# Optimization experiments

Measured on AMD Instinct MI355X. Metric: run time of the kernel, lower is better.

## Reference

```python
import jax, jax.numpy as jnp
import numpy as np

N_ATOMS = 10000
N_EDGES = 250000
F_DIM = 128
N_RBF = 20
CUTOFF = 5.0
N_INT = 3
EPS = 1e-8


def setup_inputs() -> dict:
    key = jax.random.key(0)
    ks = jax.random.split(key, 16)
    inp = {}
    inp["atomic_numbers"] = jax.random.randint(ks[0], (N_ATOMS,), 1, 101)
    # positions in a 5 Angstrom box so many pairs lie inside the cutoff
    inp["R"] = jax.random.uniform(ks[1], (N_ATOMS, 3), dtype=jnp.float32) * 5.0
    idx_i = jnp.sort(jax.random.randint(ks[2], (N_EDGES,), 0, N_ATOMS))
    # ensure idx_j != idx_i so d_ij > 0
    idx_j = (idx_i + 1 + jax.random.randint(ks[3], (N_EDGES,), 0, N_ATOMS - 1)) % N_ATOMS
    inp["idx_i"] = idx_i
    inp["idx_j"] = idx_j
    inp["offsets"] = jnp.zeros((N_EDGES, 3), dtype=jnp.float32)

    def w(k, shape):
        fan_in = shape[-2]
        return jax.random.normal(k, shape, dtype=jnp.float32) / np.sqrt(fan_in).astype(np.float32)

    inp["emb"] = jax.random.normal(ks[4], (101, F_DIM), dtype=jnp.float32)
    inp["filt_W"] = w(ks[5], (N_RBF, 3 * F_DIM))
    inp["filt_b"] = jax.random.normal(ks[6], (3 * F_DIM,), dtype=jnp.float32) * 0.01
    inp["int_W1"] = w(ks[7], (N_INT, F_DIM, F_DIM))
    inp["int_b1"] = jnp.zeros((N_INT, 1, F_DIM), dtype=jnp.float32)
    inp["int_W2"] = w(ks[8], (N_INT, F_DIM, 3 * F_DIM))
    inp["int_b2"] = jnp.zeros((N_INT, 1, 3 * F_DIM), dtype=jnp.float32)
    inp["mix_Wmu"] = w(ks[9], (N_INT, F_DIM, 2 * F_DIM))
    inp["mix_W1"] = w(ks[10], (N_INT, 2 * F_DIM, F_DIM))
    inp["mix_b1"] = jnp.zeros((N_INT, 1, F_DIM), dtype=jnp.float32)
    inp["mix_W2"] = w(ks[11], (N_INT, F_DIM, 3 * F_DIM))
    inp["mix_b2"] = jnp.zeros((N_INT, 1, 3 * F_DIM), dtype=jnp.float32)
    return inp


def painn_forward(atomic_numbers, idx_i, idx_j, R, offsets, emb, filt_W, filt_b,
                  int_W1, int_b1, int_W2, int_b2,
                  mix_Wmu, mix_W1, mix_b1, mix_W2, mix_b2):
    n_atoms = atomic_numbers.shape[0]
    # geometry
    r_ij = R[idx_j] - R[idx_i] + offsets                      # [E,3]
    d_ij = jnp.linalg.norm(r_ij, axis=1, keepdims=True)       # [E,1]
    dir_ij = r_ij / d_ij                                      # [E,3]
    # Gaussian radial basis + cosine cutoff (schnetpack defaults)
    centers = jnp.linspace(0.0, CUTOFF, N_RBF, dtype=jnp.float32)
    coeff = -0.5 / (centers[1] - centers[0]) ** 2
    phi = jnp.exp(coeff * (d_ij[..., None] - centers) ** 2)   # [E,1,N_RBF]
    fcut = 0.5 * (jnp.cos(d_ij * (jnp.pi / CUTOFF)) + 1.0) * (d_ij < CUTOFF)  # [E,1]
    Wij = (phi @ filt_W + filt_b) * fcut[..., None]           # [E,1,3F] (shared filters)

    q = emb[atomic_numbers][:, None, :]                       # [N,1,F]
    mu = jnp.zeros((n_atoms, 3, F_DIM), dtype=q.dtype)        # [N,3,F]

    for i in range(N_INT):
        # ---- interaction (equivariant message passing) ----
        x = jax.nn.silu(q @ int_W1[i] + int_b1[i]) @ int_W2[i] + int_b2[i]  # [N,1,3F]
        xj = x[idx_j]                                          # [E,1,3F]
        muj = mu[idx_j]                                        # [E,3,F]
        xw = Wij * xj                                          # [E,1,3F]
        dq, dmuR, dmumu = jnp.split(xw, 3, axis=-1)            # each [E,1,F]
        dq = jax.ops.segment_sum(dq, idx_i, num_segments=n_atoms)          # [N,1,F]
        dmu = dmuR * dir_ij[..., None] + dmumu * muj           # [E,3,F]
        dmu = jax.ops.segment_sum(dmu, idx_i, num_segments=n_atoms)        # [N,3,F]
        q = q + dq
        mu = mu + dmu
        # ---- mixing (intra-atomic) ----
        mu_mix = mu @ mix_Wmu[i]                               # [N,3,2F]
        mu_V, mu_W = jnp.split(mu_mix, 2, axis=-1)             # [N,3,F] each
        mu_Vn = jnp.sqrt(jnp.sum(mu_V ** 2, axis=-2, keepdims=True) + EPS)  # [N,1,F]
        ctx = jnp.concatenate([q, mu_Vn], axis=-1)             # [N,1,2F]
        xm = jax.nn.silu(ctx @ mix_W1[i] + mix_b1[i]) @ mix_W2[i] + mix_b2[i]  # [N,1,3F]
        dq_intra, dmu_intra, dqmu_intra = jnp.split(xm, 3, axis=-1)
        dmu_intra = dmu_intra * mu_W                           # [N,3,F]
        dqmu_intra = dqmu_intra * jnp.sum(mu_V * mu_W, axis=1, keepdims=True)  # [N,1,F]
        q = q + dq_intra + dqmu_intra
        mu = mu + dmu_intra

    return q.squeeze(1), mu                                    # [N,F], [N,3,F]


def reference(atomic_numbers, R, idx_i, idx_j, offsets, emb, filt_W, filt_b,
              int_W1, int_b1, int_W2, int_b2,
              mix_Wmu, mix_W1, mix_b1, mix_W2, mix_b2):
    return painn_forward(atomic_numbers, idx_i, idx_j, R, offsets, emb, filt_W, filt_b,
                         int_W1, int_b1, int_W2, int_b2,
                         mix_Wmu, mix_W1, mix_b1, mix_W2, mix_b2)
```

## Files before the change

### kernel.cpp

```cpp
#include <hip/hip_runtime.h>
#include <math.h>

#define NA 10000
#define NE 250000
#define FD 128
#define NRBF 20
#define RCUT 5.0f

typedef _Float16 h16;
typedef __attribute__((ext_vector_type(8))) _Float16 half8;
typedef __attribute__((ext_vector_type(2))) _Float16 half2v;
typedef __attribute__((ext_vector_type(4))) float f32x4;

static __device__ __forceinline__ half8 f32x8_to_h8(const float* p) {
    float4 a = *(const float4*)p;
    float4 b = *(const float4*)(p + 4);
    half8 r;
    r[0] = (h16)a.x; r[1] = (h16)a.y; r[2] = (h16)a.z; r[3] = (h16)a.w;
    r[4] = (h16)b.x; r[5] = (h16)b.y; r[6] = (h16)b.z; r[7] = (h16)b.w;
    return r;
}
static __device__ __forceinline__ float silu(float v) {
    return v / (1.f + expf(-v));
}

__global__ __launch_bounds__(256) void setup_kernel(
    const float* __restrict__ R, const int* __restrict__ idx_i,
    const int* __restrict__ idx_j, const float* __restrict__ offsets,
    float* __restrict__ dir, h16* __restrict__ ph, int* __restrict__ row_start,
    const float* __restrict__ int_W1, const float* __restrict__ int_W2,
    const float* __restrict__ mix_Wmu, const float* __restrict__ mix_W1,
    const float* __restrict__ mix_W2,
    h16* __restrict__ W1t, h16* __restrict__ W2t, h16* __restrict__ WmuT,
    h16* __restrict__ mW1t, h16* __restrict__ mW2t,
    const float* __restrict__ filt_W, const float* __restrict__ filt_b,
    h16* __restrict__ fwt)
{
    const int b = blockIdx.x;
    if (b < 977) {
        int e = b * 256 + threadIdx.x;
        if (e >= NE) return;
        int i = idx_i[e], j = idx_j[e];
        float rx = R[j * 3 + 0] - R[i * 3 + 0] + offsets[e * 3 + 0];
        float ry = R[j * 3 + 1] - R[i * 3 + 1] + offsets[e * 3 + 1];
        float rz = R[j * 3 + 2] - R[i * 3 + 2] + offsets[e * 3 + 2];
        float d = sqrtf(rx * rx + ry * ry + rz * rz);
        float inv = 1.f / d;
        float fcut = 0.f;
        if (d < RCUT) fcut = 0.5f * (cosf(d * (3.14159265358979323846f / RCUT)) + 1.f);
        *(float4*)&dir[(size_t)e * 4] = make_float4(rx * inv, ry * inv, rz * inv, 0.f);
        h16* pp = ph + (size_t)e * 32;
        const float delta = RCUT / 19.f;
        const float coeff = -0.5f / (delta * delta);
#pragma unroll
        for (int r = 0; r < NRBF; ++r) {
            float dc = d - (float)r * delta;
            pp[r] = (h16)(expf(coeff * dc * dc) * fcut);
        }
        pp[20] = (h16)fcut;
#pragma unroll
        for (int r = 21; r < 32; ++r) pp[r] = (h16)0.f;
    } else if (b < 1017) {
        int n = (b - 977) * 256 + threadIdx.x;
        if (n > NA) return;
        int lo = 0, hi = NE;
        while (lo < hi) {
            int mid = (lo + hi) >> 1;
            if (idx_i[mid] < n) lo = mid + 1; else hi = mid;
        }
        row_start[n] = lo;
    } else {
        int idx = (b - 1017) * 256 + threadIdx.x;
        if (idx < 49152) {
            int bt = idx >> 14, rem = idx & 16383;
            int nn = rem >> 7, kk = rem & 127;
            W1t[idx] = (h16)int_W1[(size_t)bt * 16384 + kk * 128 + nn];
        } else if ((idx -= 49152) < 147456) {
            int bt = idx / 49152, rem = idx - bt * 49152;
            int nn = rem >> 7, kk = rem & 127;
            W2t[idx] = (h16)int_W2[(size_t)bt * 49152 + kk * 384 + nn];
        } else if ((idx -= 147456) < 98304) {
            int bt = idx >> 15, rem = idx & 32767;
            int nn = rem >> 7, kk = rem & 127;
            WmuT[idx] = (h16)mix_Wmu[(size_t)bt * 32768 + kk * 256 + nn];
        } else if ((idx -= 98304) < 98304) {
            int bt = idx >> 15, rem = idx & 32767;
            int nn = rem >> 8, kk = rem & 255;
            mW1t[idx] = (h16)mix_W1[(size_t)bt * 32768 + kk * 128 + nn];
        } else if ((idx -= 98304) < 147456) {
            int bt = idx / 49152, rem = idx - bt * 49152;
            int nn = rem >> 7, kk = rem & 127;
            mW2t[idx] = (h16)mix_W2[(size_t)bt * 49152 + kk * 384 + nn];
        } else if ((idx -= 147456) < 12288) {
            int nn = idx >> 5, kk = idx & 31;
            float v = 0.f;
            if (kk < 20) v = filt_W[kk * 384 + nn];
            else if (kk == 20) v = filt_b[nn];
            fwt[idx] = (h16)v;
        }
    }
}

__global__ __launch_bounds__(256) void intmlp0_kernel(
    const int* __restrict__ Z, const float* __restrict__ emb, float* __restrict__ q,
    const h16* __restrict__ W1t, const float* __restrict__ b1,
    const h16* __restrict__ W2t, const float* __restrict__ b2, h16* __restrict__ x16)
{
    __shared__ h16 Hs[16 * 136];
    const int tid = threadIdx.x;
    const int wave = tid >> 6, lane = tid & 63;
    const int ar = lane & 15, kg = lane >> 4;
    const size_t row0 = (size_t)blockIdx.x * 16;

    {
        int a = tid >> 4, f0 = (tid & 15) * 8;
        const float* src = emb + (size_t)Z[row0 + a] * 128 + f0;
        float4 v0 = *(const float4*)src;
        float4 v1 = *(const float4*)(src + 4);
        *(float4*)&q[(row0 + a) * 128 + f0] = v0;
        *(float4*)&q[(row0 + a) * 128 + f0 + 4] = v1;
    }
    const int zr = Z[row0 + ar];
    f32x4 a1[2] = {};
    for (int ks = 0; ks < 128; ks += 32) {
        int k = ks + kg * 8;
        half8 af = f32x8_to_h8(emb + (size_t)zr * 128 + k);
#pragma unroll
        for (int tt = 0; tt < 2; ++tt) {
            int t = wave * 2 + tt;
            half8 bf = *(const half8*)&W1t[(size_t)(t * 16 + ar) * 128 + k];
            a1[tt] = __builtin_amdgcn_mfma_f32_16x16x32_f16(af, bf, a1[tt], 0, 0, 0);
        }
    }
#pragma unroll
    for (int tt = 0; tt < 2; ++tt) {
        int col = (wave * 2 + tt) * 16 + ar;
        float bb = b1[col];
#pragma unroll
        for (int r = 0; r < 4; ++r)
            Hs[(kg * 4 + r) * 136 + col] = (h16)silu(a1[tt][r] + bb);
    }
    __syncthreads();
    f32x4 a2[6] = {};
    for (int ks = 0; ks < 128; ks += 32) {
        int k = ks + kg * 8;
        half8 af = *(const half8*)&Hs[ar * 136 + k];
#pragma unroll
        for (int tt = 0; tt < 6; ++tt) {
            int t = wave * 6 + tt;
            half8 bf = *(const half8*)&W2t[(size_t)(t * 16 + ar) * 128 + k];
            a2[tt] = __builtin_amdgcn_mfma_f32_16x16x32_f16(af, bf, a2[tt], 0, 0, 0);
        }
    }
#pragma unroll
    for (int tt = 0; tt < 6; ++tt) {
        int col = (wave * 6 + tt) * 16 + ar;
        float bb = b2[col];
#pragma unroll
        for (int r = 0; r < 4; ++r)
            x16[(row0 + kg * 4 + r) * 384 + col] = (h16)(a2[tt][r] + bb);
    }
}

template<bool HAS_MU>
__global__ __launch_bounds__(128) void edge_kernel(
    const float* __restrict__ dir, const h16* __restrict__ ph,
    const h16* __restrict__ fwt,
    const int* __restrict__ row_start, const int* __restrict__ idx_j,
    const h16* __restrict__ x16, const h16* __restrict__ mu16p,
    const float* __restrict__ mup, float* __restrict__ mun,
    h16* __restrict__ mu16n, float* __restrict__ q)
{
    const int n = blockIdx.x, f = threadIdx.x;
    half2v fa[12], fb[12], fc[12];
    {
        const half8* pa = (const half8*)(fwt + (size_t)f * 32);
        const half8* pb = (const half8*)(fwt + (size_t)(128 + f) * 32);
#pragma unroll
        for (int r = 0; r < 3; ++r) {
            *(half8*)&fa[r * 4] = pa[r];
            *(half8*)&fb[r * 4] = pb[r];
        }
        if (HAS_MU) {
            const half8* pc = (const half8*)(fwt + (size_t)(256 + f) * 32);
#pragma unroll
            for (int r = 0; r < 3; ++r)
                *(half8*)&fc[r * 4] = pc[r];
        }
    }
    float accq = 0.f, am0 = 0.f, am1 = 0.f, am2 = 0.f;
    const int e0 = row_start[n], e1 = row_start[n + 1];
    for (int e = e0; e < e1; ++e) {
        half2v pr[12];
        const h16* pb8 = ph + (size_t)e * 32;
        *(half8*)&pr[0] = *(const half8*)pb8;
        *(half8*)&pr[4] = *(const half8*)(pb8 + 8);
        *(half8*)&pr[8] = *(const half8*)(pb8 + 16);
        half2v A0 = {(h16)0.f, (h16)0.f}, A1 = A0, A2 = A0;
#pragma unroll
        for (int r = 0; r < 11; ++r) {
            A0 = pr[r] * fa[r] + A0;
            A1 = pr[r] * fb[r] + A1;
            if (HAS_MU) A2 = pr[r] * fc[r] + A2;
        }
        float w0 = (float)A0[0] + (float)A0[1];
        float w1 = (float)A1[0] + (float)A1[1];
        int j = idx_j[e];
        float4 g = *(const float4*)&dir[(size_t)e * 4];
        const h16* xb = x16 + (size_t)j * 384;
        float x0 = (float)xb[f], x1 = (float)xb[128 + f];
        accq = fmaf(w0, x0, accq);
        float xw1 = w1 * x1;
        if (HAS_MU) {
            float w2 = (float)A2[0] + (float)A2[1];
            float x2 = (float)xb[256 + f];
            float xw2 = w2 * x2;
            const h16* mb = mu16p + (size_t)j * 384;
            am0 += xw1 * g.x + xw2 * (float)mb[f];
            am1 += xw1 * g.y + xw2 * (float)mb[128 + f];
            am2 += xw1 * g.z + xw2 * (float)mb[256 + f];
        } else {
            am0 = fmaf(xw1, g.x, am0);
            am1 = fmaf(xw1, g.y, am1);
            am2 = fmaf(xw1, g.z, am2);
        }
    }
    q[(size_t)n * FD + f] += accq;
    size_t b = (size_t)n * 384;
    float m0 = (HAS_MU ? mup[b + f] : 0.f) + am0;
    float m1 = (HAS_MU ? mup[b + 128 + f] : 0.f) + am1;
    float m2 = (HAS_MU ? mup[b + 256 + f] : 0.f) + am2;
    mun[b + f] = m0; mun[b + 128 + f] = m1; mun[b + 256 + f] = m2;
    mu16n[b + f] = (h16)m0; mu16n[b + 128 + f] = (h16)m1; mu16n[b + 256 + f] = (h16)m2;
}

__global__ __launch_bounds__(256) void mixint_kernel(
    const h16* __restrict__ mu16n, const h16* __restrict__ WmuT,
    const h16* __restrict__ W1t, const float* __restrict__ b1,
    const h16* __restrict__ W2t, const float* __restrict__ b2,
    float* __restrict__ q, float* __restrict__ mu, h16* __restrict__ mu16w,
    const h16* __restrict__ nW1t, const float* __restrict__ nb1,
    const h16* __restrict__ nW2t, const float* __restrict__ nb2,
    h16* __restrict__ x16)
{
    __shared__ h16 MM[48 * 264];
    __shared__ h16 CT[16 * 264];
    __shared__ h16 Hs[16 * 136];
    __shared__ h16 XM[16 * 392];
    const int tid = threadIdx.x;
    const int wave = tid >> 6, lane = tid & 63;
    const int ar = lane & 15, kg = lane >> 4;
    const size_t row0 = (size_t)blockIdx.x * 16;

    {
        f32x4 acc[3][4] = {};
        int aloc[3], dloc[3];
#pragma unroll
        for (int rt = 0; rt < 3; ++rt) {
            int rr = rt * 16 + ar;
            aloc[rt] = rr / 3;
            dloc[rt] = rr - 3 * aloc[rt];
        }
        for (int ks = 0; ks < 128; ks += 32) {
            int k = ks + kg * 8;
            half8 afr[3];
#pragma unroll
            for (int rt = 0; rt < 3; ++rt)
                afr[rt] = *(const half8*)&mu16n[(row0 + aloc[rt]) * 384 + dloc[rt] * 128 + k];
#pragma unroll
            for (int ct = 0; ct < 4; ++ct) {
                int cc = wave * 4 + ct;
                half8 bf = *(const half8*)&WmuT[(size_t)(cc * 16 + ar) * 128 + k];
#pragma unroll
                for (int rt = 0; rt < 3; ++rt)
                    acc[rt][ct] = __builtin_amdgcn_mfma_f32_16x16x32_f16(afr[rt], bf, acc[rt][ct], 0, 0, 0);
            }
        }
#pragma unroll
        for (int rt = 0; rt < 3; ++rt)
#pragma unroll
            for (int ct = 0; ct < 4; ++ct) {
                int col = (wave * 4 + ct) * 16 + ar;
#pragma unroll
                for (int r = 0; r < 4; ++r)
                    MM[(rt * 16 + kg * 4 + r) * 264 + col] = (h16)acc[rt][ct][r];
            }
    }
    __syncthreads();

    {
        int a = tid >> 4, fi = (tid & 15) * 8;
        const float* qp = q + (row0 + a) * 128 + fi;
        float4 q0 = *(const float4*)qp;
        float4 q1 = *(const float4*)(qp + 4);
        float qv[8] = {q0.x, q0.y, q0.z, q0.w, q1.x, q1.y, q1.z, q1.w};
#pragma unroll
        for (int jj = 0; jj < 8; ++jj) {
            int ff = fi + jj;
            float v0 = (float)MM[(a * 3 + 0) * 264 + ff];
            float v1 = (float)MM[(a * 3 + 1) * 264 + ff];
            float v2 = (float)MM[(a * 3 + 2) * 264 + ff];
            CT[a * 264 + 128 + ff] = (h16)sqrtf(v0 * v0 + v1 * v1 + v2 * v2 + 1e-8f);
            CT[a * 264 + ff] = (h16)qv[jj];
        }
    }
    __syncthreads();

    {
        f32x4 a1[2] = {};
        for (int ks = 0; ks < 256; ks += 32) {
            int k = ks + kg * 8;
            half8 af = *(const half8*)&CT[ar * 264 + k];
#pragma unroll
            for (int tt = 0; tt < 2; ++tt) {
                int t = wave * 2 + tt;
                half8 bf = *(const half8*)&W1t[(size_t)(t * 16 + ar) * 256 + k];
                a1[tt] = __builtin_amdgcn_mfma_f32_16x16x32_f16(af, bf, a1[tt], 0, 0, 0);
            }
        }
#pragma unroll
        for (int tt = 0; tt < 2; ++tt) {
            int col = (wave * 2 + tt) * 16 + ar;
            float bb = b1[col];
#pragma unroll
            for (int r = 0; r < 4; ++r)
                Hs[(kg * 4 + r) * 136 + col] = (h16)silu(a1[tt][r] + bb);
        }
    }
    __syncthreads();

    {
        f32x4 a2[6] = {};
        for (int ks = 0; ks < 128; ks += 32) {
            int k = ks + kg * 8;
            half8 af = *(const half8*)&Hs[ar * 136 + k];
#pragma unroll
            for (int tt = 0; tt < 6; ++tt) {
                int t = wave * 6 + tt;
                half8 bf = *(const half8*)&W2t[(size_t)(t * 16 + ar) * 128 + k];
                a2[tt] = __builtin_amdgcn_mfma_f32_16x16x32_f16(af, bf, a2[tt], 0, 0, 0);
            }
        }
#pragma unroll
        for (int tt = 0; tt < 6; ++tt) {
            int col = (wave * 6 + tt) * 16 + ar;
            float bb = b2[col];
#pragma unroll
            for (int r = 0; r < 4; ++r)
                XM[(kg * 4 + r) * 392 + col] = (h16)(a2[tt][r] + bb);
        }
    }
    __syncthreads();

    {
        int a = tid >> 4, fi = (tid & 15) * 8;
        size_t n = row0 + a;
#pragma unroll
        for (int jj = 0; jj < 8; ++jj) {
            int ff = fi + jj;
            float dq  = (float)XM[a * 392 + ff];
            float dm  = (float)XM[a * 392 + 128 + ff];
            float dqm = (float)XM[a * 392 + 256 + ff];
            float v0 = (float)MM[(a * 3 + 0) * 264 + ff], w0 = (float)MM[(a * 3 + 0) * 264 + 128 + ff];
            float v1 = (float)MM[(a * 3 + 1) * 264 + ff], w1 = (float)MM[(a * 3 + 1) * 264 + 128 + ff];
            float v2 = (float)MM[(a * 3 + 2) * 264 + ff], w2 = (float)MM[(a * 3 + 2) * 264 + 128 + ff];
            float sv = v0 * w0 + v1 * w1 + v2 * w2;
            float qn = q[n * 128 + ff] + dq + dqm * sv;
            q[n * 128 + ff] = qn;
            CT[a * 264 + ff] = (h16)qn;
            size_t b = n * 384 + ff;
            float m0 = mu[b] + dm * w0;
            float m1 = mu[b + 128] + dm * w1;
            float m2 = mu[b + 256] + dm * w2;
            mu[b] = m0; mu[b + 128] = m1; mu[b + 256] = m2;
            mu16w[b] = (h16)m0; mu16w[b + 128] = (h16)m1; mu16w[b + 256] = (h16)m2;
        }
    }
    if (!nW1t) return;
    __syncthreads();

    {
        f32x4 a1[2] = {};
        for (int ks = 0; ks < 128; ks += 32) {
            int k = ks + kg * 8;
            half8 af = *(const half8*)&CT[ar * 264 + k];
#pragma unroll
            for (int tt = 0; tt < 2; ++tt) {
                int t = wave * 2 + tt;
                half8 bf = *(const half8*)&nW1t[(size_t)(t * 16 + ar) * 128 + k];
                a1[tt] = __builtin_amdgcn_mfma_f32_16x16x32_f16(af, bf, a1[tt], 0, 0, 0);
            }
        }
#pragma unroll
        for (int tt = 0; tt < 2; ++tt) {
            int col = (wave * 2 + tt) * 16 + ar;
            float bb = nb1[col];
#pragma unroll
            for (int r = 0; r < 4; ++r)
                Hs[(kg * 4 + r) * 136 + col] = (h16)silu(a1[tt][r] + bb);
        }
        __syncthreads();
        f32x4 a2[6] = {};
        for (int ks = 0; ks < 128; ks += 32) {
            int k = ks + kg * 8;
            half8 af = *(const half8*)&Hs[ar * 136 + k];
#pragma unroll
            for (int tt = 0; tt < 6; ++tt) {
                int t = wave * 6 + tt;
                half8 bf = *(const half8*)&nW2t[(size_t)(t * 16 + ar) * 128 + k];
                a2[tt] = __builtin_amdgcn_mfma_f32_16x16x32_f16(af, bf, a2[tt], 0, 0, 0);
            }
        }
#pragma unroll
        for (int tt = 0; tt < 6; ++tt) {
            int col = (wave * 6 + tt) * 16 + ar;
            float bb = nb2[col];
#pragma unroll
            for (int r = 0; r < 4; ++r)
                x16[(row0 + kg * 4 + r) * 384 + col] = (h16)(a2[tt][r] + bb);
        }
    }
}

extern "C" void kernel_launch(void* const* d_in, const int* in_sizes, int n_in,
                              void* d_out, int out_size, void* d_ws, size_t ws_size,
                              hipStream_t stream)
{
    const int*   Z       = (const int*)d_in[0];
    const float* R       = (const float*)d_in[1];
    const int*   idx_i   = (const int*)d_in[2];
    const int*   idx_j   = (const int*)d_in[3];
    const float* offsets = (const float*)d_in[4];
    const float* emb     = (const float*)d_in[5];
    const float* filt_W  = (const float*)d_in[6];
    const float* filt_b  = (const float*)d_in[7];
    const float* int_W1  = (const float*)d_in[8];
    const float* int_b1  = (const float*)d_in[9];
    const float* int_W2  = (const float*)d_in[10];
    const float* int_b2  = (const float*)d_in[11];
    const float* mix_Wmu = (const float*)d_in[12];
    const float* mix_W1  = (const float*)d_in[13];
    const float* mix_b1  = (const float*)d_in[14];
    const float* mix_W2  = (const float*)d_in[15];
    const float* mix_b2  = (const float*)d_in[16];

    float* q_out  = (float*)d_out;
    float* mu_out = (float*)d_out + (size_t)NA * FD;

    char* base = (char*)d_ws;
    size_t o = 0;
    auto alloc = [&](size_t bytes) -> void* {
        void* p = base + o;
        o += (bytes + 255) & ~(size_t)255;
        return p;
    };
    float* dir    = (float*)alloc((size_t)NE * 4 * 4);
    h16*   ph     = (h16*)alloc((size_t)NE * 32 * 2);
    h16*   x16    = (h16*)alloc((size_t)NA * 384 * 2);
    h16*   mu16a  = (h16*)alloc((size_t)NA * 384 * 2);
    h16*   mu16b  = (h16*)alloc((size_t)NA * 384 * 2);
    float* mu_ws  = (float*)alloc((size_t)NA * 384 * 4);
    h16*   W1t    = (h16*)alloc((size_t)3 * 128 * 128 * 2);
    h16*   W2t    = (h16*)alloc((size_t)3 * 384 * 128 * 2);
    h16*   WmuT   = (h16*)alloc((size_t)3 * 256 * 128 * 2);
    h16*   mW1t   = (h16*)alloc((size_t)3 * 128 * 256 * 2);
    h16*   mW2t   = (h16*)alloc((size_t)3 * 384 * 128 * 2);
    h16*   fwt    = (h16*)alloc((size_t)384 * 32 * 2);
    int*   row_st = (int*)alloc((size_t)(NA + 1) * 4);

    setup_kernel<<<3177, 256, 0, stream>>>(R, idx_i, idx_j, offsets, dir, ph, row_st,
                                           int_W1, int_W2, mix_Wmu, mix_W1, mix_W2,
                                           W1t, W2t, WmuT, mW1t, mW2t,
                                           filt_W, filt_b, fwt);

    intmlp0_kernel<<<NA / 16, 256, 0, stream>>>(Z, emb, q_out,
                                                W1t, int_b1, W2t, int_b2, x16);
    edge_kernel<false><<<NA, 128, 0, stream>>>(dir, ph, fwt, row_st, idx_j,
                                               x16, nullptr, nullptr, mu_out, mu16b, q_out);
    mixint_kernel<<<NA / 16, 256, 0, stream>>>(
        mu16b, WmuT, mW1t, mix_b1, mW2t, mix_b2, q_out, mu_out, mu16b,
        W1t + 16384, int_b1 + 128, W2t + 49152, int_b2 + 384, x16);

    edge_kernel<true><<<NA, 128, 0, stream>>>(dir, ph, fwt, row_st, idx_j,
                                              x16, mu16b, mu_out, mu_ws, mu16a, q_out);
    mixint_kernel<<<NA / 16, 256, 0, stream>>>(
        mu16a, WmuT + 32768, mW1t + 32768, mix_b1 + 128, mW2t + 49152, mix_b2 + 384,
        q_out, mu_ws, mu16a,
        W1t + 32768, int_b1 + 256, W2t + 98304, int_b2 + 768, x16);

    edge_kernel<true><<<NA, 128, 0, stream>>>(dir, ph, fwt, row_st, idx_j,
                                              x16, mu16a, mu_ws, mu_out, mu16b, q_out);
    mixint_kernel<<<NA / 16, 256, 0, stream>>>(
        mu16b, WmuT + 65536, mW1t + 65536, mix_b1 + 256, mW2t + 98304, mix_b2 + 768,
        q_out, mu_out, mu16b,
        nullptr, nullptr, nullptr, nullptr, nullptr);
}
```

Before: 443.8 us.

## Prune out-of-cutoff edges into compact CSR and interleave x/mu gather layout

Edges with distance at or beyond the cutoff are dropped during setup, and surviving edges are compacted per source atom with atomic counters, storing their neighbour index. A separate kernel computes row starts and clears the counters. Edge kernels iterate only over surviving edges and gather x and mu from one interleaved per-(atom, feature) 6-half record, not from three separate strided arrays. This trades nondeterministic edge order within a row and strided stores for fewer edges processed and fewer gather loads.

Result: slower. 545.7 us (+23.0%).

```diff
diff --git a/kernel.cpp b/kernel.cpp
--- a/kernel.cpp
+++ b/kernel.cpp
@@ -24,10 +24,25 @@
     return v / (1.f + expf(-v));
 }
 
+__global__ void csr_kernel(const int* __restrict__ idx_i, int* __restrict__ row_start,
+                           int* __restrict__ cnt)
+{
+    int n = blockIdx.x * 256 + threadIdx.x;
+    if (n > NA) return;
+    int lo = 0, hi = NE;
+    while (lo < hi) {
+        int mid = (lo + hi) >> 1;
+        if (idx_i[mid] < n) lo = mid + 1; else hi = mid;
+    }
+    row_start[n] = lo;
+    if (n < NA) cnt[n] = 0;
+}
+
 __global__ __launch_bounds__(256) void setup_kernel(
     const float* __restrict__ R, const int* __restrict__ idx_i,
     const int* __restrict__ idx_j, const float* __restrict__ offsets,
-    float* __restrict__ dir, h16* __restrict__ ph, int* __restrict__ row_start,
+    float* __restrict__ dir, h16* __restrict__ ph, int* __restrict__ jdx,
+    const int* __restrict__ row_start, int* __restrict__ cnt,
     const float* __restrict__ int_W1, const float* __restrict__ int_W2,
     const float* __restrict__ mix_Wmu, const float* __restrict__ mix_W1,
     const float* __restrict__ mix_W2,
@@ -45,11 +60,14 @@
         float ry = R[j * 3 + 1] - R[i * 3 + 1] + offsets[e * 3 + 1];
         float rz = R[j * 3 + 2] - R[i * 3 + 2] + offsets[e * 3 + 2];
         float d = sqrtf(rx * rx + ry * ry + rz * rz);
+        if (d >= RCUT) return;
         float inv = 1.f / d;
-        float fcut = 0.f;
-        if (d < RCUT) fcut = 0.5f * (cosf(d * (3.14159265358979323846f / RCUT)) + 1.f);
-        *(float4*)&dir[(size_t)e * 4] = make_float4(rx * inv, ry * inv, rz * inv, 0.f);
-        h16* pp = ph + (size_t)e * 32;
+        float fcut = 0.5f * (cosf(d * (3.14159265358979323846f / RCUT)) + 1.f);
+        int pos = atomicAdd(&cnt[i], 1);
+        int s = row_start[i] + pos;
+        *(float4*)&dir[(size_t)s * 4] = make_float4(rx * inv, ry * inv, rz * inv, 0.f);
+        jdx[s] = j;
+        h16* pp = ph + (size_t)s * 32;
         const float delta = RCUT / 19.f;
         const float coeff = -0.5f / (delta * delta);
 #pragma unroll
@@ -60,17 +78,8 @@
         pp[20] = (h16)fcut;
 #pragma unroll
         for (int r = 21; r < 32; ++r) pp[r] = (h16)0.f;
-    } else if (b < 1017) {
-        int n = (b - 977) * 256 + threadIdx.x;
-        if (n > NA) return;
-        int lo = 0, hi = NE;
-        while (lo < hi) {
-            int mid = (lo + hi) >> 1;
-            if (idx_i[mid] < n) lo = mid + 1; else hi = mid;
-        }
-        row_start[n] = lo;
     } else {
-        int idx = (b - 1017) * 256 + threadIdx.x;
+        int idx = (b - 977) * 256 + threadIdx.x;
         if (idx < 49152) {
             int bt = idx >> 14, rem = idx & 16383;
             int nn = rem >> 7, kk = rem & 127;
@@ -104,7 +113,7 @@
 __global__ __launch_bounds__(256) void intmlp0_kernel(
     const int* __restrict__ Z, const float* __restrict__ emb, float* __restrict__ q,
     const h16* __restrict__ W1t, const float* __restrict__ b1,
-    const h16* __restrict__ W2t, const float* __restrict__ b2, h16* __restrict__ x16)
+    const h16* __restrict__ W2t, const float* __restrict__ b2, h16* __restrict__ xm)
 {
     __shared__ h16 Hs[16 * 136];
     const int tid = threadIdx.x;
@@ -155,10 +164,11 @@
 #pragma unroll
     for (int tt = 0; tt < 6; ++tt) {
         int col = (wave * 6 + tt) * 16 + ar;
+        int cm = col & 127, cs = col >> 7;
         float bb = b2[col];
 #pragma unroll
         for (int r = 0; r < 4; ++r)
-            x16[(row0 + kg * 4 + r) * 384 + col] = (h16)(a2[tt][r] + bb);
+            xm[((row0 + kg * 4 + r) * 128 + cm) * 6 + cs] = (h16)(a2[tt][r] + bb);
     }
 }
 
@@ -166,8 +176,8 @@
 __global__ __launch_bounds__(128) void edge_kernel(
     const float* __restrict__ dir, const h16* __restrict__ ph,
     const h16* __restrict__ fwt,
-    const int* __restrict__ row_start, const int* __restrict__ idx_j,
-    const h16* __restrict__ x16, const h16* __restrict__ mu16p,
+    const int* __restrict__ row_start, const int* __restrict__ cnt,
+    const int* __restrict__ jdx, const h16* __restrict__ xm,
     const float* __restrict__ mup, float* __restrict__ mun,
     h16* __restrict__ mu16n, float* __restrict__ q)
 {
@@ -189,7 +199,7 @@
         }
     }
     float accq = 0.f, am0 = 0.f, am1 = 0.f, am2 = 0.f;
-    const int e0 = row_start[n], e1 = row_start[n + 1];
+    const int e0 = row_start[n], e1 = e0 + cnt[n];
     for (int e = e0; e < e1; ++e) {
         half2v pr[12];
         const h16* pb8 = ph + (size_t)e * 32;
@@ -205,20 +215,22 @@
         }
         float w0 = (float)A0[0] + (float)A0[1];
         float w1 = (float)A1[0] + (float)A1[1];
-        int j = idx_j[e];
+        int j = jdx[e];
         float4 g = *(const float4*)&dir[(size_t)e * 4];
-        const h16* xb = x16 + (size_t)j * 384;
-        float x0 = (float)xb[f], x1 = (float)xb[128 + f];
+        const h16* xb = xm + ((size_t)j * 128 + f) * 6;
+        half2v d0 = *(const half2v*)xb;
+        half2v d1 = *(const half2v*)(xb + 2);
+        float x0 = (float)d0[0], x1 = (float)d0[1];
         accq = fmaf(w0, x0, accq);
         float xw1 = w1 * x1;
         if (HAS_MU) {
+            half2v d2 = *(const half2v*)(xb + 4);
             float w2 = (float)A2[0] + (float)A2[1];
-            float x2 = (float)xb[256 + f];
+            float x2 = (float)d1[0];
             float xw2 = w2 * x2;
-            const h16* mb = mu16p + (size_t)j * 384;
-            am0 += xw1 * g.x + xw2 * (float)mb[f];
-            am1 += xw1 * g.y + xw2 * (float)mb[128 + f];
-            am2 += xw1 * g.z + xw2 * (float)mb[256 + f];
+            am0 += xw1 * g.x + xw2 * (float)d1[1];
+            am1 += xw1 * g.y + xw2 * (float)d2[0];
+            am2 += xw1 * g.z + xw2 * (float)d2[1];
         } else {
             am0 = fmaf(xw1, g.x, am0);
             am1 = fmaf(xw1, g.y, am1);
@@ -238,10 +250,9 @@
     const h16* __restrict__ mu16n, const h16* __restrict__ WmuT,
     const h16* __restrict__ W1t, const float* __restrict__ b1,
     const h16* __restrict__ W2t, const float* __restrict__ b2,
-    float* __restrict__ q, float* __restrict__ mu, h16* __restrict__ mu16w,
+    float* __restrict__ q, float* __restrict__ mu, h16* __restrict__ xmw,
     const h16* __restrict__ nW1t, const float* __restrict__ nb1,
-    const h16* __restrict__ nW2t, const float* __restrict__ nb2,
-    h16* __restrict__ x16)
+    const h16* __restrict__ nW2t, const float* __restrict__ nb2)
 {
     __shared__ h16 MM[48 * 264];
     __shared__ h16 CT[16 * 264];
@@ -373,7 +384,10 @@
             float m1 = mu[b + 128] + dm * w1;
             float m2 = mu[b + 256] + dm * w2;
             mu[b] = m0; mu[b + 128] = m1; mu[b + 256] = m2;
-            mu16w[b] = (h16)m0; mu16w[b + 128] = (h16)m1; mu16w[b + 256] = (h16)m2;
+            if (xmw) {
+                h16* xw = xmw + (n * 128 + ff) * 6;
+                xw[3] = (h16)m0; xw[4] = (h16)m1; xw[5] = (h16)m2;
+            }
         }
     }
     if (!nW1t) return;
@@ -414,10 +428,11 @@
 #pragma unroll
         for (int tt = 0; tt < 6; ++tt) {
             int col = (wave * 6 + tt) * 16 + ar;
+            int cm = col & 127, cs = col >> 7;
             float bb = nb2[col];
 #pragma unroll
             for (int r = 0; r < 4; ++r)
-                x16[(row0 + kg * 4 + r) * 384 + col] = (h16)(a2[tt][r] + bb);
+                xmw[((row0 + kg * 4 + r) * 128 + cm) * 6 + cs] = (h16)(a2[tt][r] + bb);
         }
     }
 }
@@ -456,9 +471,10 @@
     };
     float* dir    = (float*)alloc((size_t)NE * 4 * 4);
     h16*   ph     = (h16*)alloc((size_t)NE * 32 * 2);
-    h16*   x16    = (h16*)alloc((size_t)NA * 384 * 2);
-    h16*   mu16a  = (h16*)alloc((size_t)NA * 384 * 2);
-    h16*   mu16b  = (h16*)alloc((size_t)NA * 384 * 2);
+    int*   jdx    = (int*)alloc((size_t)NE * 4);
+    h16*   xmA    = (h16*)alloc((size_t)NA * 128 * 6 * 2);
+    h16*   xmB    = (h16*)alloc((size_t)NA * 128 * 6 * 2);
+    h16*   mu16c  = (h16*)alloc((size_t)NA * 384 * 2);
     float* mu_ws  = (float*)alloc((size_t)NA * 384 * 4);
     h16*   W1t    = (h16*)alloc((size_t)3 * 128 * 128 * 2);
     h16*   W2t    = (h16*)alloc((size_t)3 * 384 * 128 * 2);
@@ -467,31 +483,34 @@
     h16*   mW2t   = (h16*)alloc((size_t)3 * 384 * 128 * 2);
     h16*   fwt    = (h16*)alloc((size_t)384 * 32 * 2);
     int*   row_st = (int*)alloc((size_t)(NA + 1) * 4);
-
-    setup_kernel<<<3177, 256, 0, stream>>>(R, idx_i, idx_j, offsets, dir, ph, row_st,
+    int*   cnt    = (int*)alloc((size_t)NA * 4);
+
+    csr_kernel<<<(NA + 256) / 256, 256, 0, stream>>>(idx_i, row_st, cnt);
+    setup_kernel<<<3137, 256, 0, stream>>>(R, idx_i, idx_j, offsets, dir, ph, jdx,
+                                           row_st, cnt,
                                            int_W1, int_W2, mix_Wmu, mix_W1, mix_W2,
                                            W1t, W2t, WmuT, mW1t, mW2t,
                                            filt_W, filt_b, fwt);
 
     intmlp0_kernel<<<NA / 16, 256, 0, stream>>>(Z, emb, q_out,
-                                                W1t, int_b1, W2t, int_b2, x16);
-    edge_kernel<false><<<NA, 128, 0, stream>>>(dir, ph, fwt, row_st, idx_j,
-                                               x16, nullptr, nullptr, mu_out, mu16b, q_out);
+                                                W1t, int_b1, W2t, int_b2, xmA);
+    edge_kernel<false><<<NA, 128, 0, stream>>>(dir, ph, fwt, row_st, cnt, jdx,
+                                               xmA, nullptr, mu_out, mu16c, q_out);
     mixint_kernel<<<NA / 16, 256, 0, stream>>>(
-        mu16b, WmuT, mW1t, mix_b1, mW2t, mix_b2, q_out, mu_out, mu16b,
-        W1t + 16384, int_b1 + 128, W2t + 49152, int_b2 + 384, x16);
-
-    edge_kernel<true><<<NA, 128, 0, stream>>>(dir, ph, fwt, row_st, idx_j,
-                                              x16, mu16b, mu_out, mu_ws, mu16a, q_out);
+        mu16c, WmuT, mW1t, mix_b1, mW2t, mix_b2, q_out, mu_out, xmB,
+        W1t + 16384, int_b1 + 128, W2t + 49152, int_b2 + 384);
+
+    edge_kernel<true><<<NA, 128, 0, stream>>>(dir, ph, fwt, row_st, cnt, jdx,
+                                              xmB, mu_out, mu_ws, mu16c, q_out);
     mixint_kernel<<<NA / 16, 256, 0, stream>>>(
-        mu16a, WmuT + 32768, mW1t + 32768, mix_b1 + 128, mW2t + 49152, mix_b2 + 384,
-        q_out, mu_ws, mu16a,
-        W1t + 32768, int_b1 + 256, W2t + 98304, int_b2 + 768, x16);
-
-    edge_kernel<true><<<NA, 128, 0, stream>>>(dir, ph, fwt, row_st, idx_j,
-                                              x16, mu16a, mu_ws, mu_out, mu16b, q_out);
+        mu16c, WmuT + 32768, mW1t + 32768, mix_b1 + 128, mW2t + 49152, mix_b2 + 384,
+        q_out, mu_ws, xmA,
+        W1t + 32768, int_b1 + 256, W2t + 98304, int_b2 + 768);
+
+    edge_kernel<true><<<NA, 128, 0, stream>>>(dir, ph, fwt, row_st, cnt, jdx,
+                                              xmA, mu_ws, mu_out, mu16c, q_out);
     mixint_kernel<<<NA / 16, 256, 0, stream>>>(
-        mu16b, WmuT + 65536, mW1t + 65536, mix_b1 + 256, mW2t + 98304, mix_b2 + 768,
-        q_out, mu_out, mu16b,
-        nullptr, nullptr, nullptr, nullptr, nullptr);
-}
+        mu16c, WmuT + 65536, mW1t + 65536, mix_b1 + 256, mW2t + 98304, mix_b2 + 768,
+        q_out, mu_out, nullptr,
+        nullptr, nullptr, nullptr, nullptr);
+}
```

## Compact in-cutoff edges per atom and fuse mix MLP epilogue into MFMA outputs

Applied to the files above, without the earlier changes.

Edges with distance beyond the cutoff contribute zero and are now discarded in setup. The remaining edges are compacted per atom into a CSR layout using atomic counters, so the edge kernels iterate only over contributing neighbours. The CSR row starts move into a separate kernel. The mixing kernel's second GEMM is reorganised so each wave computes matching dq/dmu/dqmu columns and applies the update directly from registers, dropping a shared buffer and a barrier. Atomic slot assignment makes the per-atom edge summation order nondeterministic.

Result: slower. 478.4 us (+7.8%).

```diff
diff --git a/kernel.cpp b/kernel.cpp
--- a/kernel.cpp
+++ b/kernel.cpp
@@ -24,10 +24,25 @@
     return v / (1.f + expf(-v));
 }
 
+__global__ void csr_kernel(const int* __restrict__ idx_i, int* __restrict__ row_start,
+                           int* __restrict__ cnt)
+{
+    int n = blockIdx.x * 256 + threadIdx.x;
+    if (n > NA) return;
+    int lo = 0, hi = NE;
+    while (lo < hi) {
+        int mid = (lo + hi) >> 1;
+        if (idx_i[mid] < n) lo = mid + 1; else hi = mid;
+    }
+    row_start[n] = lo;
+    if (n < NA) cnt[n] = 0;
+}
+
 __global__ __launch_bounds__(256) void setup_kernel(
     const float* __restrict__ R, const int* __restrict__ idx_i,
     const int* __restrict__ idx_j, const float* __restrict__ offsets,
-    float* __restrict__ dir, h16* __restrict__ ph, int* __restrict__ row_start,
+    float* __restrict__ dir, h16* __restrict__ ph, int* __restrict__ jdx,
+    const int* __restrict__ row_start, int* __restrict__ cnt,
     const float* __restrict__ int_W1, const float* __restrict__ int_W2,
     const float* __restrict__ mix_Wmu, const float* __restrict__ mix_W1,
     const float* __restrict__ mix_W2,
@@ -45,11 +60,14 @@
         float ry = R[j * 3 + 1] - R[i * 3 + 1] + offsets[e * 3 + 1];
         float rz = R[j * 3 + 2] - R[i * 3 + 2] + offsets[e * 3 + 2];
         float d = sqrtf(rx * rx + ry * ry + rz * rz);
+        if (d >= RCUT) return;
         float inv = 1.f / d;
-        float fcut = 0.f;
-        if (d < RCUT) fcut = 0.5f * (cosf(d * (3.14159265358979323846f / RCUT)) + 1.f);
-        *(float4*)&dir[(size_t)e * 4] = make_float4(rx * inv, ry * inv, rz * inv, 0.f);
-        h16* pp = ph + (size_t)e * 32;
+        float fcut = 0.5f * (cosf(d * (3.14159265358979323846f / RCUT)) + 1.f);
+        int pos = atomicAdd(&cnt[i], 1);
+        int s = row_start[i] + pos;
+        *(float4*)&dir[(size_t)s * 4] = make_float4(rx * inv, ry * inv, rz * inv, 0.f);
+        jdx[s] = j;
+        h16* pp = ph + (size_t)s * 32;
         const float delta = RCUT / 19.f;
         const float coeff = -0.5f / (delta * delta);
 #pragma unroll
@@ -60,17 +78,8 @@
         pp[20] = (h16)fcut;
 #pragma unroll
         for (int r = 21; r < 32; ++r) pp[r] = (h16)0.f;
-    } else if (b < 1017) {
-        int n = (b - 977) * 256 + threadIdx.x;
-        if (n > NA) return;
-        int lo = 0, hi = NE;
-        while (lo < hi) {
-            int mid = (lo + hi) >> 1;
-            if (idx_i[mid] < n) lo = mid + 1; else hi = mid;
-        }
-        row_start[n] = lo;
     } else {
-        int idx = (b - 1017) * 256 + threadIdx.x;
+        int idx = (b - 977) * 256 + threadIdx.x;
         if (idx < 49152) {
             int bt = idx >> 14, rem = idx & 16383;
             int nn = rem >> 7, kk = rem & 127;
@@ -166,7 +175,8 @@
 __global__ __launch_bounds__(128) void edge_kernel(
     const float* __restrict__ dir, const h16* __restrict__ ph,
     const h16* __restrict__ fwt,
-    const int* __restrict__ row_start, const int* __restrict__ idx_j,
+    const int* __restrict__ row_start, const int* __restrict__ cnt,
+    const int* __restrict__ jdx,
     const h16* __restrict__ x16, const h16* __restrict__ mu16p,
     const float* __restrict__ mup, float* __restrict__ mun,
     h16* __restrict__ mu16n, float* __restrict__ q)
@@ -189,7 +199,7 @@
         }
     }
     float accq = 0.f, am0 = 0.f, am1 = 0.f, am2 = 0.f;
-    const int e0 = row_start[n], e1 = row_start[n + 1];
+    const int e0 = row_start[n], e1 = e0 + cnt[n];
     for (int e = e0; e < e1; ++e) {
         half2v pr[12];
         const h16* pb8 = ph + (size_t)e * 32;
@@ -205,7 +215,7 @@
         }
         float w0 = (float)A0[0] + (float)A0[1];
         float w1 = (float)A1[0] + (float)A1[1];
-        int j = idx_j[e];
+        int j = jdx[e];
         float4 g = *(const float4*)&dir[(size_t)e * 4];
         const h16* xb = x16 + (size_t)j * 384;
         float x0 = (float)xb[f], x1 = (float)xb[128 + f];
@@ -246,7 +256,6 @@
     __shared__ h16 MM[48 * 264];
     __shared__ h16 CT[16 * 264];
     __shared__ h16 Hs[16 * 136];
-    __shared__ h16 XM[16 * 392];
     const int tid = threadIdx.x;
     const int wave = tid >> 6, lane = tid & 63;
     const int ar = lane & 15, kg = lane >> 4;
@@ -329,46 +338,41 @@
     }
     __syncthreads();
 
-    {
-        f32x4 a2[6] = {};
-        for (int ks = 0; ks < 128; ks += 32) {
-            int k = ks + kg * 8;
-            half8 af = *(const half8*)&Hs[ar * 136 + k];
-#pragma unroll
-            for (int tt = 0; tt < 6; ++tt) {
-                int t = wave * 6 + tt;
-                half8 bf = *(const half8*)&W2t[(size_t)(t * 16 + ar) * 128 + k];
-                a2[tt] = __builtin_amdgcn_mfma_f32_16x16x32_f16(af, bf, a2[tt], 0, 0, 0);
-            }
-        }
-#pragma unroll
-        for (int tt = 0; tt < 6; ++tt) {
-            int col = (wave * 6 + tt) * 16 + ar;
-            float bb = b2[col];
-#pragma unroll
-            for (int r = 0; r < 4; ++r)
-                XM[(kg * 4 + r) * 392 + col] = (h16)(a2[tt][r] + bb);
-        }
-    }
-    __syncthreads();
-
-    {
-        int a = tid >> 4, fi = (tid & 15) * 8;
-        size_t n = row0 + a;
-#pragma unroll
-        for (int jj = 0; jj < 8; ++jj) {
-            int ff = fi + jj;
-            float dq  = (float)XM[a * 392 + ff];
-            float dm  = (float)XM[a * 392 + 128 + ff];
-            float dqm = (float)XM[a * 392 + 256 + ff];
-            float v0 = (float)MM[(a * 3 + 0) * 264 + ff], w0 = (float)MM[(a * 3 + 0) * 264 + 128 + ff];
-            float v1 = (float)MM[(a * 3 + 1) * 264 + ff], w1 = (float)MM[(a * 3 + 1) * 264 + 128 + ff];
-            float v2 = (float)MM[(a * 3 + 2) * 264 + ff], w2 = (float)MM[(a * 3 + 2) * 264 + 128 + ff];
+    f32x4 aq[2] = {}, am[2] = {}, ag[2] = {};
+    for (int ks = 0; ks < 128; ks += 32) {
+        int k = ks + kg * 8;
+        half8 af = *(const half8*)&Hs[ar * 136 + k];
+#pragma unroll
+        for (int p = 0; p < 2; ++p) {
+            int t = wave * 2 + p;
+            half8 bq = *(const half8*)&W2t[(size_t)(t * 16 + ar) * 128 + k];
+            aq[p] = __builtin_amdgcn_mfma_f32_16x16x32_f16(af, bq, aq[p], 0, 0, 0);
+            half8 bm = *(const half8*)&W2t[(size_t)((8 + t) * 16 + ar) * 128 + k];
+            am[p] = __builtin_amdgcn_mfma_f32_16x16x32_f16(af, bm, am[p], 0, 0, 0);
+            half8 bg = *(const half8*)&W2t[(size_t)((16 + t) * 16 + ar) * 128 + k];
+            ag[p] = __builtin_amdgcn_mfma_f32_16x16x32_f16(af, bg, ag[p], 0, 0, 0);
+        }
+    }
+
+#pragma unroll
+    for (int p = 0; p < 2; ++p) {
+        int f = (wave * 2 + p) * 16 + ar;
+        float bdq = b2[f], bdm = b2[128 + f], bdg = b2[256 + f];
+#pragma unroll
+        for (int r = 0; r < 4; ++r) {
+            int aL = kg * 4 + r;
+            size_t n = row0 + aL;
+            float dq  = aq[p][r] + bdq;
+            float dm  = am[p][r] + bdm;
+            float dqm = ag[p][r] + bdg;
+            float v0 = (float)MM[(aL * 3 + 0) * 264 + f], w0 = (float)MM[(aL * 3 + 0) * 264 + 128 + f];
+            float v1 = (float)MM[(aL * 3 + 1) * 264 + f], w1 = (float)MM[(aL * 3 + 1) * 264 + 128 + f];
+            float v2 = (float)MM[(aL * 3 + 2) * 264 + f], w2 = (float)MM[(aL * 3 + 2) * 264 + 128 + f];
             float sv = v0 * w0 + v1 * w1 + v2 * w2;
-            float qn = q[n * 128 + ff] + dq + dqm * sv;
-            q[n * 128 + ff] = qn;
-            CT[a * 264 + ff] = (h16)qn;
-            size_t b = n * 384 + ff;
+            float qn = q[n * 128 + f] + dq + dqm * sv;
+            q[n * 128 + f] = qn;
+            CT[aL * 264 + f] = (h16)qn;
+            size_t b = n * 384 + f;
             float m0 = mu[b] + dm * w0;
             float m1 = mu[b + 128] + dm * w1;
             float m2 = mu[b + 256] + dm * w2;
@@ -456,6 +460,7 @@
     };
     float* dir    = (float*)alloc((size_t)NE * 4 * 4);
     h16*   ph     = (h16*)alloc((size_t)NE * 32 * 2);
+    int*   jdx    = (int*)alloc((size_t)NE * 4);
     h16*   x16    = (h16*)alloc((size_t)NA * 384 * 2);
     h16*   mu16a  = (h16*)alloc((size_t)NA * 384 * 2);
     h16*   mu16b  = (h16*)alloc((size_t)NA * 384 * 2);
@@ -467,28 +472,31 @@
     h16*   mW2t   = (h16*)alloc((size_t)3 * 384 * 128 * 2);
     h16*   fwt    = (h16*)alloc((size_t)384 * 32 * 2);
     int*   row_st = (int*)alloc((size_t)(NA + 1) * 4);
-
-    setup_kernel<<<3177, 256, 0, stream>>>(R, idx_i, idx_j, offsets, dir, ph, row_st,
+    int*   cnt    = (int*)alloc((size_t)NA * 4);
+
+    csr_kernel<<<(NA + 256) / 256, 256, 0, stream>>>(idx_i, row_st, cnt);
+    setup_kernel<<<3137, 256, 0, stream>>>(R, idx_i, idx_j, offsets, dir, ph, jdx,
+                                           row_st, cnt,
                                            int_W1, int_W2, mix_Wmu, mix_W1, mix_W2,
                                            W1t, W2t, WmuT, mW1t, mW2t,
                                            filt_W, filt_b, fwt);
 
     intmlp0_kernel<<<NA / 16, 256, 0, stream>>>(Z, emb, q_out,
                                                 W1t, int_b1, W2t, int_b2, x16);
-    edge_kernel<false><<<NA, 128, 0, stream>>>(dir, ph, fwt, row_st, idx_j,
+    edge_kernel<false><<<NA, 128, 0, stream>>>(dir, ph, fwt, row_st, cnt, jdx,
                                                x16, nullptr, nullptr, mu_out, mu16b, q_out);
     mixint_kernel<<<NA / 16, 256, 0, stream>>>(
         mu16b, WmuT, mW1t, mix_b1, mW2t, mix_b2, q_out, mu_out, mu16b,
         W1t + 16384, int_b1 + 128, W2t + 49152, int_b2 + 384, x16);
 
-    edge_kernel<true><<<NA, 128, 0, stream>>>(dir, ph, fwt, row_st, idx_j,
+    edge_kernel<true><<<NA, 128, 0, stream>>>(dir, ph, fwt, row_st, cnt, jdx,
                                               x16, mu16b, mu_out, mu_ws, mu16a, q_out);
     mixint_kernel<<<NA / 16, 256, 0, stream>>>(
         mu16a, WmuT + 32768, mW1t + 32768, mix_b1 + 128, mW2t + 49152, mix_b2 + 384,
         q_out, mu_ws, mu16a,
         W1t + 32768, int_b1 + 256, W2t + 98304, int_b2 + 768, x16);
 
-    edge_kernel<true><<<NA, 128, 0, stream>>>(dir, ph, fwt, row_st, idx_j,
+    edge_kernel<true><<<NA, 128, 0, stream>>>(dir, ph, fwt, row_st, cnt, jdx,
                                               x16, mu16a, mu_ws, mu_out, mu16b, q_out);
     mixint_kernel<<<NA / 16, 256, 0, stream>>>(
         mu16b, WmuT + 65536, mW1t + 65536, mix_b1 + 256, mW2t + 98304, mix_b2 + 768,
```

## Compact edges inside cutoff into per-atom CSR to skip zero-contribution edges

Applied to the files above, without the earlier changes.

Setup now drops edges whose distance is at or beyond the cutoff, since their cutoff weight is zero. Surviving edges are written compactly into each atom's CSR segment using an atomic counter, along with a new compacted neighbor-index array. The edge kernels then loop only over the per-atom count. This adds a separate CSR kernel launch and atomics, and makes the edge order inside each atom, and so the float summation order, nondeterministic.

After: 473.6 us. 1.07x slower.

```diff
diff --git a/kernel.cpp b/kernel.cpp
--- a/kernel.cpp
+++ b/kernel.cpp
@@ -24,10 +24,25 @@
     return v / (1.f + expf(-v));
 }
 
+__global__ void csr_kernel(const int* __restrict__ idx_i, int* __restrict__ row_start,
+                           int* __restrict__ cnt)
+{
+    int n = blockIdx.x * 256 + threadIdx.x;
+    if (n > NA) return;
+    int lo = 0, hi = NE;
+    while (lo < hi) {
+        int mid = (lo + hi) >> 1;
+        if (idx_i[mid] < n) lo = mid + 1; else hi = mid;
+    }
+    row_start[n] = lo;
+    if (n < NA) cnt[n] = 0;
+}
+
 __global__ __launch_bounds__(256) void setup_kernel(
     const float* __restrict__ R, const int* __restrict__ idx_i,
     const int* __restrict__ idx_j, const float* __restrict__ offsets,
-    float* __restrict__ dir, h16* __restrict__ ph, int* __restrict__ row_start,
+    float* __restrict__ dir, h16* __restrict__ ph, int* __restrict__ jdx,
+    const int* __restrict__ row_start, int* __restrict__ cnt,
     const float* __restrict__ int_W1, const float* __restrict__ int_W2,
     const float* __restrict__ mix_Wmu, const float* __restrict__ mix_W1,
     const float* __restrict__ mix_W2,
@@ -45,11 +60,14 @@
         float ry = R[j * 3 + 1] - R[i * 3 + 1] + offsets[e * 3 + 1];
         float rz = R[j * 3 + 2] - R[i * 3 + 2] + offsets[e * 3 + 2];
         float d = sqrtf(rx * rx + ry * ry + rz * rz);
+        if (d >= RCUT) return;
         float inv = 1.f / d;
-        float fcut = 0.f;
-        if (d < RCUT) fcut = 0.5f * (cosf(d * (3.14159265358979323846f / RCUT)) + 1.f);
-        *(float4*)&dir[(size_t)e * 4] = make_float4(rx * inv, ry * inv, rz * inv, 0.f);
-        h16* pp = ph + (size_t)e * 32;
+        float fcut = 0.5f * (cosf(d * (3.14159265358979323846f / RCUT)) + 1.f);
+        int pos = atomicAdd(&cnt[i], 1);
+        int s = row_start[i] + pos;
+        *(float4*)&dir[(size_t)s * 4] = make_float4(rx * inv, ry * inv, rz * inv, 0.f);
+        jdx[s] = j;
+        h16* pp = ph + (size_t)s * 32;
         const float delta = RCUT / 19.f;
         const float coeff = -0.5f / (delta * delta);
 #pragma unroll
@@ -60,17 +78,8 @@
         pp[20] = (h16)fcut;
 #pragma unroll
         for (int r = 21; r < 32; ++r) pp[r] = (h16)0.f;
-    } else if (b < 1017) {
-        int n = (b - 977) * 256 + threadIdx.x;
-        if (n > NA) return;
-        int lo = 0, hi = NE;
-        while (lo < hi) {
-            int mid = (lo + hi) >> 1;
-            if (idx_i[mid] < n) lo = mid + 1; else hi = mid;
-        }
-        row_start[n] = lo;
     } else {
-        int idx = (b - 1017) * 256 + threadIdx.x;
+        int idx = (b - 977) * 256 + threadIdx.x;
         if (idx < 49152) {
             int bt = idx >> 14, rem = idx & 16383;
             int nn = rem >> 7, kk = rem & 127;
@@ -166,7 +175,8 @@
 __global__ __launch_bounds__(128) void edge_kernel(
     const float* __restrict__ dir, const h16* __restrict__ ph,
     const h16* __restrict__ fwt,
-    const int* __restrict__ row_start, const int* __restrict__ idx_j,
+    const int* __restrict__ row_start, const int* __restrict__ cnt,
+    const int* __restrict__ jdx,
     const h16* __restrict__ x16, const h16* __restrict__ mu16p,
     const float* __restrict__ mup, float* __restrict__ mun,
     h16* __restrict__ mu16n, float* __restrict__ q)
@@ -189,7 +199,7 @@
         }
     }
     float accq = 0.f, am0 = 0.f, am1 = 0.f, am2 = 0.f;
-    const int e0 = row_start[n], e1 = row_start[n + 1];
+    const int e0 = row_start[n], e1 = e0 + cnt[n];
     for (int e = e0; e < e1; ++e) {
         half2v pr[12];
         const h16* pb8 = ph + (size_t)e * 32;
@@ -205,7 +215,7 @@
         }
         float w0 = (float)A0[0] + (float)A0[1];
         float w1 = (float)A1[0] + (float)A1[1];
-        int j = idx_j[e];
+        int j = jdx[e];
         float4 g = *(const float4*)&dir[(size_t)e * 4];
         const h16* xb = x16 + (size_t)j * 384;
         float x0 = (float)xb[f], x1 = (float)xb[128 + f];
@@ -456,6 +466,7 @@
     };
     float* dir    = (float*)alloc((size_t)NE * 4 * 4);
     h16*   ph     = (h16*)alloc((size_t)NE * 32 * 2);
+    int*   jdx    = (int*)alloc((size_t)NE * 4);
     h16*   x16    = (h16*)alloc((size_t)NA * 384 * 2);
     h16*   mu16a  = (h16*)alloc((size_t)NA * 384 * 2);
     h16*   mu16b  = (h16*)alloc((size_t)NA * 384 * 2);
@@ -467,28 +478,31 @@
     h16*   mW2t   = (h16*)alloc((size_t)3 * 384 * 128 * 2);
     h16*   fwt    = (h16*)alloc((size_t)384 * 32 * 2);
     int*   row_st = (int*)alloc((size_t)(NA + 1) * 4);
-
-    setup_kernel<<<3177, 256, 0, stream>>>(R, idx_i, idx_j, offsets, dir, ph, row_st,
+    int*   cnt    = (int*)alloc((size_t)NA * 4);
+
+    csr_kernel<<<(NA + 256) / 256, 256, 0, stream>>>(idx_i, row_st, cnt);
+    setup_kernel<<<3137, 256, 0, stream>>>(R, idx_i, idx_j, offsets, dir, ph, jdx,
+                                           row_st, cnt,
                                            int_W1, int_W2, mix_Wmu, mix_W1, mix_W2,
                                            W1t, W2t, WmuT, mW1t, mW2t,
                                            filt_W, filt_b, fwt);
 
     intmlp0_kernel<<<NA / 16, 256, 0, stream>>>(Z, emb, q_out,
                                                 W1t, int_b1, W2t, int_b2, x16);
-    edge_kernel<false><<<NA, 128, 0, stream>>>(dir, ph, fwt, row_st, idx_j,
+    edge_kernel<false><<<NA, 128, 0, stream>>>(dir, ph, fwt, row_st, cnt, jdx,
                                                x16, nullptr, nullptr, mu_out, mu16b, q_out);
     mixint_kernel<<<NA / 16, 256, 0, stream>>>(
         mu16b, WmuT, mW1t, mix_b1, mW2t, mix_b2, q_out, mu_out, mu16b,
         W1t + 16384, int_b1 + 128, W2t + 49152, int_b2 + 384, x16);
 
-    edge_kernel<true><<<NA, 128, 0, stream>>>(dir, ph, fwt, row_st, idx_j,
+    edge_kernel<true><<<NA, 128, 0, stream>>>(dir, ph, fwt, row_st, cnt, jdx,
                                               x16, mu16b, mu_out, mu_ws, mu16a, q_out);
     mixint_kernel<<<NA / 16, 256, 0, stream>>>(
         mu16a, WmuT + 32768, mW1t + 32768, mix_b1 + 128, mW2t + 49152, mix_b2 + 384,
         q_out, mu_ws, mu16a,
         W1t + 32768, int_b1 + 256, W2t + 98304, int_b2 + 768, x16);
 
-    edge_kernel<true><<<NA, 128, 0, stream>>>(dir, ph, fwt, row_st, idx_j,
+    edge_kernel<true><<<NA, 128, 0, stream>>>(dir, ph, fwt, row_st, cnt, jdx,
                                               x16, mu16a, mu_ws, mu_out, mu16b, q_out);
     mixint_kernel<<<NA / 16, 256, 0, stream>>>(
         mu16b, WmuT + 65536, mW1t + 65536, mix_b1 + 256, mW2t + 98304, mix_b2 + 768,
```
